# Kernel optimization log

Measured on AMD Instinct MI355X. Metric: run time of the kernel, lower is better.

## Reference

```python
import jax, jax.numpy as jnp
import numpy as np
from jax import lax

BITS = 8
STRIDE = 1
PADDING = 1
SCALE = 2.0 ** (BITS - 1)  # fixed-point scale 2^(bits-1)


def setup_inputs() -> dict:
    key = jax.random.key(0)
    k1, k2, k3 = jax.random.split(key, 3)
    x = jax.random.normal(k1, (32, 128, 56, 56), dtype=jnp.float32)
    W = jax.random.normal(k2, (256, 128, 3, 3), dtype=jnp.float32)
    b = jax.random.normal(k3, (256,), dtype=jnp.float32)
    return {"x": x, "W": W, "b": b}


def reference(x, W, b):
    # to_fix_point: round(v * 2^(bits-1)); torch keeps long ints, but all
    # arithmetic in forward promotes back to float, so float round is exact here.
    w_q = jnp.round(W * SCALE)
    b_q = jnp.round(b * SCALE)
    # calConv: out[i,j] = sum(patch * w_q) / 2^(bits-1) + b_q
    # (square 3x3 kernel makes the original's transposed patch indexing a standard conv)
    out = lax.conv_general_dilated(
        x, w_q,
        window_strides=(STRIDE, STRIDE),
        padding=[(PADDING, PADDING), (PADDING, PADDING)],
        dimension_numbers=("NCHW", "OIHW", "NCHW"),
    )
    return out / SCALE + b_q[None, :, None, None]
```

## Files before the change

### kernel.cpp

```cpp
#include <hip/hip_runtime.h>

typedef _Float16 half8 __attribute__((ext_vector_type(8)));
typedef float floatx4 __attribute__((ext_vector_type(4)));

#define IMG   3136
#define PIMG  3364
#define XP_ELEMS (32 * 58 * 58 * 128)
#define WQ_ELEMS (9 * 256 * 128)

#define AS1 __attribute__((address_space(1)))
#define AS3 __attribute__((address_space(3)))

__global__ __launch_bounds__(256) void pad_x_kernel(const float* __restrict__ x,
                                                    _Float16* __restrict__ xp) {
    const int hh = blockIdx.x;
    const int n  = blockIdx.y;
    const int t  = threadIdx.x;
    _Float16* rowbase = xp + ((long)(n * 58 + hh) * 58) * 128;

    if (hh == 0 || hh == 57) {
        #pragma unroll
        for (int i = 0; i < 4; ++i) {
            int idx = i * 256 + t;
            if (idx < 928) *(half8*)(rowbase + idx * 8) = (half8)(_Float16)0.0f;
        }
        return;
    }

    __shared__ _Float16 tile[128 * 57];
    const int h = hh - 1;

    #pragma unroll
    for (int p = 0; p < 7; ++p) {
        int idx = p * 256 + t;
        int c   = idx / 14;
        int w4  = (idx % 14) * 4;
        const float4 v = *(const float4*)(x + ((long)(n * 128 + c) * 56 + h) * 56 + w4);
        _Float16* d = tile + c * 57 + w4;
        d[0] = (_Float16)v.x; d[1] = (_Float16)v.y;
        d[2] = (_Float16)v.z; d[3] = (_Float16)v.w;
    }
    __syncthreads();

    #pragma unroll
    for (int p = 0; p < 4; ++p) {
        int idx = p * 256 + t;
        if (idx < 896) {
            int ww = idx >> 4;
            int c0 = (idx & 15) * 8;
            half8 v;
            #pragma unroll
            for (int j = 0; j < 8; ++j) v[j] = tile[(c0 + j) * 57 + ww];
            *(half8*)(rowbase + (ww + 1) * 128 + c0) = v;
        }
    }
    if (t < 32) {
        int ww = (t >> 4) ? 57 : 0;
        int c0 = (t & 15) * 8;
        *(half8*)(rowbase + ww * 128 + c0) = (half8)(_Float16)0.0f;
    }
}

__global__ void quant_w_kernel(const float* __restrict__ W, _Float16* __restrict__ wq) {
    int t = blockIdx.x * 256 + threadIdx.x;
    int c  = t & 127;
    int k  = (t >> 7) & 255;
    int rs = t >> 15;
    wq[t] = (_Float16)rintf(W[(k * 128 + c) * 9 + rs] * 128.0f);
}

__global__ __launch_bounds__(256) void conv_mfma_kernel(
    const _Float16* __restrict__ xp, const _Float16* __restrict__ wq,
    const float* __restrict__ b, float* __restrict__ out)
{
    __shared__ __align__(16) _Float16 smem[16384];

    const int tid = threadIdx.x;
    const int l   = tid & 63;
    const int wv  = tid >> 6;
    const int wm  = wv & 1;
    const int wn  = wv >> 1;
    const int bx  = blockIdx.x;
    const int by  = blockIdx.y;

    const int lrow = l >> 2;
    const int lcol = ((l & 3) ^ ((l >> 3) & 3)) * 8;

    const int aoff0 = (by * 128 + wv * 16 + lrow) * 128 + lcol;
    const int aoff1 = aoff0 + 64 * 128;

    const int pix0 = bx * 128 + wv * 16 + lrow;
    const int pix1 = pix0 + 64;
    const int n0 = pix0 / IMG, hw0 = pix0 % IMG;
    const int n1 = pix1 / IMG, hw1 = pix1 % IMG;
    const int pb0 = (n0 * PIMG + (hw0 / 56) * 58 + (hw0 % 56)) * 128 + lcol;
    const int pb1 = (n1 * PIMG + (hw1 / 56) * 58 + (hw1 % 56)) * 128 + lcol;

    const int stageoff = wv * 512;

    floatx4 acc[4][4] = {};

    auto issue = [&](int t, int pbuf) {
        const int rs = t >> 2;
        const int cc = t & 3;
        const int r  = (rs * 11) >> 5;
        const int s2 = rs - r * 3;
        const _Float16* wg = wq + rs * (256 * 128);
        const _Float16* xg = xp + (r * 58 + s2) * 128;
        const int co = cc * 32;
        _Float16* A = smem + pbuf * 8192 + stageoff;
        _Float16* B = smem + pbuf * 8192 + 4096 + stageoff;
        __builtin_amdgcn_global_load_lds((AS1 void*)(wg + aoff0 + co), (AS3 void*)A,          16, 0, 0);
        __builtin_amdgcn_global_load_lds((AS1 void*)(wg + aoff1 + co), (AS3 void*)(A + 2048), 16, 0, 0);
        __builtin_amdgcn_global_load_lds((AS1 void*)(xg + pb0  + co), (AS3 void*)B,          16, 0, 0);
        __builtin_amdgcn_global_load_lds((AS1 void*)(xg + pb1  + co), (AS3 void*)(B + 2048), 16, 0, 0);
    };

    const int ar = wm * 64 + (l & 15);
    const int br = wn * 64 + (l & 15);
    const int kq = ((l >> 4) ^ ((l >> 1) & 3)) * 8;

    auto compute = [&](int pbuf) {
        const _Float16* As = smem + pbuf * 8192;
        const _Float16* Bs = As + 4096;
        half8 af[4], bf[4];
        #pragma unroll
        for (int mi = 0; mi < 4; ++mi)
            af[mi] = *(const half8*)(As + (ar + mi * 16) * 32 + kq);
        #pragma unroll
        for (int ni = 0; ni < 4; ++ni)
            bf[ni] = *(const half8*)(Bs + (br + ni * 16) * 32 + kq);
        #pragma unroll
        for (int mi = 0; mi < 4; ++mi)
            #pragma unroll
            for (int ni = 0; ni < 4; ++ni)
                acc[mi][ni] = __builtin_amdgcn_mfma_f32_16x16x32_f16(af[mi], bf[ni], acc[mi][ni], 0, 0, 0);
    };

    issue(0, 0);
    #pragma unroll 2
    for (int s = 0; s < 35; ++s) {
        issue(s + 1, (s + 1) & 1);
        asm volatile("s_waitcnt vmcnt(4)" ::: "memory");
        asm volatile("s_barrier" ::: "memory");
        compute(s & 1);
        asm volatile("s_barrier" ::: "memory");
    }
    asm volatile("s_waitcnt vmcnt(0)" ::: "memory");
    asm volatile("s_barrier" ::: "memory");
    compute(1);

    #pragma unroll
    for (int mi = 0; mi < 4; ++mi) {
        const int kb = by * 128 + wm * 64 + mi * 16 + (l >> 4) * 4;
        #pragma unroll
        for (int rg = 0; rg < 4; ++rg) {
            const int k = kb + rg;
            const float bq = rintf(b[k] * 128.0f);
            #pragma unroll
            for (int ni = 0; ni < 4; ++ni) {
                const int pix = bx * 128 + wn * 64 + ni * 16 + (l & 15);
                const int n  = pix / IMG;
                const int pr = pix - n * IMG;
                out[((long)n * 256 + k) * IMG + pr] = acc[mi][ni][rg] * (1.0f / 128.0f) + bq;
            }
        }
    }
}

__global__ void conv_fallback_kernel(const float* __restrict__ x, const float* __restrict__ W,
                                     const float* __restrict__ b, float* __restrict__ out)
{
    __shared__ float wsm[1152];
    const int k = blockIdx.y;
    for (int i = threadIdx.x; i < 1152; i += 256)
        wsm[i] = rintf(W[k * 1152 + i] * 128.0f);
    __syncthreads();
    const int pix = blockIdx.x * 256 + threadIdx.x;
    const int n = pix / IMG, hw = pix % IMG;
    const int h = hw / 56, w = hw % 56;
    float acc = 0.0f;
    for (int c = 0; c < 128; ++c) {
        const float* xr = x + ((n * 128 + c) * 56) * 56;
        const float* wr = wsm + c * 9;
        #pragma unroll
        for (int r = 0; r < 3; ++r) {
            const int hh = h + r - 1;
            if ((unsigned)hh >= 56u) continue;
            #pragma unroll
            for (int s = 0; s < 3; ++s) {
                const int ww = w + s - 1;
                if ((unsigned)ww >= 56u) continue;
                acc += xr[hh * 56 + ww] * wr[r * 3 + s];
            }
        }
    }
    out[((long)n * 256 + k) * IMG + hw] = acc * (1.0f / 128.0f) + rintf(b[k] * 128.0f);
}

extern "C" void kernel_launch(void* const* d_in, const int* in_sizes, int n_in,
                              void* d_out, int out_size, void* d_ws, size_t ws_size,
                              hipStream_t stream) {
    const float* x = (const float*)d_in[0];
    const float* W = (const float*)d_in[1];
    const float* b = (const float*)d_in[2];
    float* out = (float*)d_out;

    const size_t need = (size_t)XP_ELEMS * 2 + (size_t)WQ_ELEMS * 2;
    if (ws_size >= need) {
        _Float16* xp = (_Float16*)d_ws;
        _Float16* wq = xp + XP_ELEMS;
        pad_x_kernel<<<dim3(58, 32), 256, 0, stream>>>(x, xp);
        quant_w_kernel<<<WQ_ELEMS / 256, 256, 0, stream>>>(W, wq);
        conv_mfma_kernel<<<dim3(784, 2), 256, 0, stream>>>(xp, wq, b, out);
    } else {
        conv_fallback_kernel<<<dim3(392, 256), 256, 0, stream>>>(x, W, b, out);
    }
}
```

Before: 212.9 us.

## Load weight fragments directly into registers instead of staging through LDS

The weight (A) operand no longer goes through shared memory. Each wave loads its MFMA A-fragments straight from global memory into a double-buffered register array, while the input (B) tile is still streamed into LDS with global_load_lds. This halves LDS usage and removes LDS reads for A. The cost is more VGPRs and uncoalesced per-lane 16-byte global loads of weights, which are redundant across the two waves sharing wm. The vmcnt wait count is raised to account for the extra outstanding loads.

```diff
diff --git a/kernel.cpp b/kernel.cpp
--- a/kernel.cpp
+++ b/kernel.cpp
@@ -73,7 +73,7 @@
     const _Float16* __restrict__ xp, const _Float16* __restrict__ wq,
     const float* __restrict__ b, float* __restrict__ out)
 {
-    __shared__ __align__(16) _Float16 smem[16384];
+    __shared__ __align__(16) _Float16 smem[8192];
 
     const int tid = threadIdx.x;
     const int l   = tid & 63;
@@ -86,9 +86,6 @@
     const int lrow = l >> 2;
     const int lcol = ((l & 3) ^ ((l >> 3) & 3)) * 8;
 
-    const int aoff0 = (by * 128 + wv * 16 + lrow) * 128 + lcol;
-    const int aoff1 = aoff0 + 64 * 128;
-
     const int pix0 = bx * 128 + wv * 16 + lrow;
     const int pix1 = pix0 + 64;
     const int n0 = pix0 / IMG, hw0 = pix0 % IMG;
@@ -98,35 +95,37 @@
 
     const int stageoff = wv * 512;
 
+    const int aBase = (by * 128 + wm * 64 + (l & 15)) * 128 + (l >> 4) * 8;
+
     floatx4 acc[4][4] = {};
 
-    auto issue = [&](int t, int pbuf) {
+    auto issueB = [&](int t, int pbuf) {
         const int rs = t >> 2;
         const int cc = t & 3;
         const int r  = (rs * 11) >> 5;
         const int s2 = rs - r * 3;
-        const _Float16* wg = wq + rs * (256 * 128);
-        const _Float16* xg = xp + (r * 58 + s2) * 128;
-        const int co = cc * 32;
-        _Float16* A = smem + pbuf * 8192 + stageoff;
-        _Float16* B = smem + pbuf * 8192 + 4096 + stageoff;
-        __builtin_amdgcn_global_load_lds((AS1 void*)(wg + aoff0 + co), (AS3 void*)A,          16, 0, 0);
-        __builtin_amdgcn_global_load_lds((AS1 void*)(wg + aoff1 + co), (AS3 void*)(A + 2048), 16, 0, 0);
-        __builtin_amdgcn_global_load_lds((AS1 void*)(xg + pb0  + co), (AS3 void*)B,          16, 0, 0);
-        __builtin_amdgcn_global_load_lds((AS1 void*)(xg + pb1  + co), (AS3 void*)(B + 2048), 16, 0, 0);
+        const _Float16* xg = xp + (r * 58 + s2) * 128 + cc * 32;
+        _Float16* B = smem + pbuf * 4096 + stageoff;
+        __builtin_amdgcn_global_load_lds((AS1 void*)(xg + pb0), (AS3 void*)B,          16, 0, 0);
+        __builtin_amdgcn_global_load_lds((AS1 void*)(xg + pb1), (AS3 void*)(B + 2048), 16, 0, 0);
     };
 
-    const int ar = wm * 64 + (l & 15);
+    half8 afA[2][4];
+    auto loadA = [&](int t, int slot) {
+        const int rs = t >> 2;
+        const int cc = t & 3;
+        const _Float16* wg = wq + rs * (256 * 128) + aBase + cc * 32;
+        #pragma unroll
+        for (int mi = 0; mi < 4; ++mi)
+            afA[slot][mi] = *(const half8*)(wg + mi * (16 * 128));
+    };
+
     const int br = wn * 64 + (l & 15);
     const int kq = ((l >> 4) ^ ((l >> 1) & 3)) * 8;
 
-    auto compute = [&](int pbuf) {
-        const _Float16* As = smem + pbuf * 8192;
-        const _Float16* Bs = As + 4096;
-        half8 af[4], bf[4];
-        #pragma unroll
-        for (int mi = 0; mi < 4; ++mi)
-            af[mi] = *(const half8*)(As + (ar + mi * 16) * 32 + kq);
+    auto compute = [&](int pbuf, int slot) {
+        const _Float16* Bs = smem + pbuf * 4096;
+        half8 bf[4];
         #pragma unroll
         for (int ni = 0; ni < 4; ++ni)
             bf[ni] = *(const half8*)(Bs + (br + ni * 16) * 32 + kq);
@@ -134,21 +133,23 @@
         for (int mi = 0; mi < 4; ++mi)
             #pragma unroll
             for (int ni = 0; ni < 4; ++ni)
-                acc[mi][ni] = __builtin_amdgcn_mfma_f32_16x16x32_f16(af[mi], bf[ni], acc[mi][ni], 0, 0, 0);
+                acc[mi][ni] = __builtin_amdgcn_mfma_f32_16x16x32_f16(afA[slot][mi], bf[ni], acc[mi][ni], 0, 0, 0);
     };
 
-    issue(0, 0);
+    issueB(0, 0);
+    loadA(0, 0);
     #pragma unroll 2
     for (int s = 0; s < 35; ++s) {
-        issue(s + 1, (s + 1) & 1);
-        asm volatile("s_waitcnt vmcnt(4)" ::: "memory");
+        issueB(s + 1, (s + 1) & 1);
+        loadA(s + 1, (s + 1) & 1);
+        asm volatile("s_waitcnt vmcnt(6)" ::: "memory");
         asm volatile("s_barrier" ::: "memory");
-        compute(s & 1);
+        compute(s & 1, s & 1);
         asm volatile("s_barrier" ::: "memory");
     }
     asm volatile("s_waitcnt vmcnt(0)" ::: "memory");
     asm volatile("s_barrier" ::: "memory");
-    compute(1);
+    compute(1, 1);
 
     #pragma unroll
     for (int mi = 0; mi < 4; ++mi) {
```

Measured after the change: 274.4 us. 1.29x slower.
